# Optimization experiments

Hardware: AMD Instinct MI355X
Metric: run time of the kernel (lower is better)

The kernel has to match this reference:

```python
import jax, jax.numpy as jnp
import numpy as np

V, NLAB, NLAYERS, DI, DM, DS, DD, K = 32000, 9, 2, 768, 1536, 16, 96, 4
B, S = 2, 2048
EPS = 1e-6


def setup_inputs() -> dict:
    key = jax.random.key(0)
    ks = jax.random.split(key, 12)
    n = lambda k, shape, s=0.02: jax.random.normal(k, shape, jnp.float32) * s
    return {
        "input_ids": jax.random.randint(ks[0], (B, S), 0, V, dtype=jnp.int32),
        "attention_mask": jnp.ones((B, S), jnp.int32),
        "emb": n(ks[1], (V, DI)),
        "norm_w": jnp.ones((NLAYERS, DI), jnp.float32),
        "in_proj_w": n(ks[2], (NLAYERS, 2 * DM, DI)),
        "conv_w": n(ks[3], (NLAYERS, DM, K), 0.1),
        "conv_b": jnp.zeros((NLAYERS, DM), jnp.float32),
        "sB_w": n(ks[4], (NLAYERS, DS, DM)),
        "sC_w": n(ks[5], (NLAYERS, DS, DM)),
        "sD1_w": n(ks[6], (NLAYERS, DD, DM)),
        "sD2_w": n(ks[7], (NLAYERS, DM, DD)),
        "A": jnp.tile(jnp.arange(1, DS + 1, dtype=jnp.float32), (NLAYERS, DM, 1)),
        "Dp": jnp.ones((NLAYERS, DM), jnp.float32),
        "out_w": n(ks[8], (NLAYERS, DI, DM)),
        "cls_w": n(ks[9], (NLAB, DI)),
        "cls_b": jnp.zeros((NLAB,), jnp.float32),
    }


def _rmsnorm(x, w):
    return x * jax.lax.rsqrt(jnp.mean(x * x, axis=-1, keepdims=True) + EPS) * w


def _mamba_block(x, norm_w, Wi, cw, cb, WB, WC, W1, W2, A, Dp, Wo):
    # x: (b, l, d_input)
    h = _rmsnorm(x, norm_w)
    a, gate = jnp.split(h @ Wi.T, 2, axis=-1)  # each (b, l, DM)
    # causal depthwise conv1d, kernel K, left-pad K-1 (== Conv1d(pad=K-1)[..., :l])
    L = a.shape[1]
    ap = jnp.pad(a, ((0, 0), (K - 1, 0), (0, 0)))
    conv = cb + sum(ap[:, i:i + L, :] * cw[:, i] for i in range(K))
    a = jax.nn.silu(conv)
    # selective SSM
    Bm = a @ WB.T                                   # (b, l, DS)
    Cm = a @ WC.T                                   # (b, l, DS)
    delta = jax.nn.softplus(Dp + (a @ W1.T) @ W2.T)  # (b, l, DM)
    A_bar = jnp.exp(delta[..., None] * (-A))         # (b, l, DM, DS)
    X_bar = (delta * a)[..., None] * Bm[:, :, None, :]  # (b, l, DM, DS)

    def comb(c1, c2):
        a1, x1 = c1
        a2, x2 = c2
        return a1 * a2, a2 * x1 + x2

    _, hid = jax.lax.associative_scan(comb, (A_bar, X_bar), axis=1)
    y = jnp.einsum('blds,bls->bld', hid, Cm) + Dp * a
    y = y * jax.nn.silu(gate)
    return y @ Wo.T


def _forward(input_ids, attention_mask, emb, norm_w, in_proj_w, conv_w, conv_b,
             sB_w, sC_w, sD1_w, sD2_w, A, Dp, out_w, cls_w, cls_b):
    x = emb[input_ids] * attention_mask[..., None].astype(emb.dtype)
    for i in range(NLAYERS):  # residual Mamba layers
        x = _mamba_block(x, norm_w[i], in_proj_w[i], conv_w[i], conv_b[i],
                         sB_w[i], sC_w[i], sD1_w[i], sD2_w[i], A[i], Dp[i], out_w[i]) + x
    # dropout is identity at inference
    return x @ cls_w.T + cls_b  # logits (b, l, num_labels)


def reference(input_ids, attention_mask, emb, norm_w, in_proj_w, conv_w, conv_b,
              sB_w, sC_w, sD1_w, sD2_w, A, Dp, out_w, cls_w, cls_b):
    return _forward(input_ids, attention_mask, emb, norm_w, in_proj_w, conv_w, conv_b,
                    sB_w, sC_w, sD1_w, sD2_w, A, Dp, out_w, cls_w, cls_b)
```

## Files before the change

kernel.cpp:

```cpp
#include <hip/hip_runtime.h>
#include <hip/hip_bf16.h>
#include <math.h>

#define NLAB 9
#define NL   2
#define DI   768
#define DM   1536
#define DS   16
#define KC   4
#define DD   96
#define BB   2
#define SS   2048
#define TT   (BB*SS)
#define EPSF 1e-6f

#define NCH  32
#define CL   (SS/NCH)

#define NW   128
#define KS   8
#define KSL  (DM/KS)

typedef __attribute__((ext_vector_type(4))) float f32x4;
typedef __attribute__((ext_vector_type(8))) short bf16x8;
typedef __attribute__((ext_vector_type(4))) unsigned short us4;
typedef __attribute__((ext_vector_type(8))) unsigned short us8;

__device__ __forceinline__ float siluf(float x) { return x / (1.f + __expf(-x)); }
__device__ __forceinline__ float softplusf(float x) { return x > 15.f ? x : log1pf(__expf(x)); }

__device__ __forceinline__ unsigned short f2bf(float f) {
    unsigned u = __float_as_uint(f);
    return (unsigned short)((u + 0x7fffu + ((u >> 16) & 1u)) >> 16);
}
__device__ __forceinline__ float bf2f(unsigned short s) {
    return __uint_as_float((unsigned)s << 16);
}

__device__ __forceinline__ void xcd_map(int gx, int gy, int bx, int by,
                                        int& bmt, int& bnt)
{
    int flat = by * gx + bx;
    if ((gx & 1) == 0 && (gy & 3) == 0) {
        int halfx = gx >> 1, quarty = gy >> 2;
        int xcd = flat & 7, local = flat >> 3;
        bnt = (xcd & 1) * halfx + local % halfx;
        bmt = (xcd >> 1) * quarty + local / halfx;
    } else { bmt = by; bnt = bx; }
}

__global__ void f32_to_bf16(const float* __restrict__ src,
                            unsigned short* __restrict__ dst, int n)
{
    int i = (blockIdx.x * 256 + threadIdx.x) * 8;
    if (i >= n) return;
    float4 a = *(const float4*)(src + i);
    float4 b = *(const float4*)(src + i + 4);
    union { unsigned short s[8]; uint4 v; } o;
    o.s[0] = f2bf(a.x); o.s[1] = f2bf(a.y); o.s[2] = f2bf(a.z); o.s[3] = f2bf(a.w);
    o.s[4] = f2bf(b.x); o.s[5] = f2bf(b.y); o.s[6] = f2bf(b.z); o.s[7] = f2bf(b.w);
    *(uint4*)(dst + i) = o.v;
}

__global__ void embed_kernel(const int* __restrict__ ids, const int* __restrict__ mask,
                             const float* __restrict__ emb, float* __restrict__ x)
{
    int t = blockIdx.x;
    int i = threadIdx.x;
    float m = (float)mask[t];
    int id = ids[t];
    float4 v = ((const float4*)(emb + (size_t)id * DI))[i];
    v.x *= m; v.y *= m; v.z *= m; v.w *= m;
    ((float4*)(x + (size_t)t * DI))[i] = v;
}

__global__ void rmsnorm_kernel(const float* __restrict__ x, const float* __restrict__ w,
                               unsigned short* __restrict__ h)
{
    __shared__ float red[4];
    int t = blockIdx.x;
    const float* xr = x + (size_t)t * DI;
    float ss = 0.f;
    for (int i = threadIdx.x; i < DI; i += 256) { float v = xr[i]; ss += v * v; }
    #pragma unroll
    for (int m = 1; m < 64; m <<= 1) ss += __shfl_xor(ss, m, 64);
    if ((threadIdx.x & 63) == 0) red[threadIdx.x >> 6] = ss;
    __syncthreads();
    float scale = rsqrtf((red[0] + red[1] + red[2] + red[3]) * (1.f / DI) + EPSF);
    for (int i = threadIdx.x; i < DI; i += 256)
        h[(size_t)t * DI + i] = f2bf(xr[i] * scale * w[i]);
}

#define STAGE_TILE(AS, BS, KT) do {                                                           \
    _Pragma("unroll")                                                                         \
    for (int it = 0; it < 2; ++it) {                                                          \
        int rbase = it * 64 + wave * 16;                                                      \
        int row = rbase + (lane >> 2);                                                        \
        int c8 = (((lane & 3) ^ ((lane >> 3) & 3)) * 8);                                      \
        __builtin_amdgcn_global_load_lds(                                                     \
            (const __attribute__((address_space(1))) unsigned int*)(Arow + (size_t)row * lda + (KT) + c8), \
            (__attribute__((address_space(3))) unsigned int*)((AS) + rbase * 32), 16, 0, 0);  \
        __builtin_amdgcn_global_load_lds(                                                     \
            (const __attribute__((address_space(1))) unsigned int*)(Brow + (size_t)row * ldb + (KT) + c8), \
            (__attribute__((address_space(3))) unsigned int*)((BS) + rbase * 32), 16, 0, 0);  \
    } } while (0)

#define COMPUTE_TILE(AS, BS) do {                                                             \
    bf16x8 af[4], bfr[4];                                                                     \
    const int khs = (kh ^ ((lr >> 1) & 3)) * 8;                                               \
    _Pragma("unroll")                                                                         \
    for (int i = 0; i < 4; ++i)                                                               \
        af[i] = *(const bf16x8*)&(AS)[(wm + i * 16 + lr) * 32 + khs];                         \
    _Pragma("unroll")                                                                         \
    for (int j = 0; j < 4; ++j)                                                               \
        bfr[j] = *(const bf16x8*)&(BS)[(wn + j * 16 + lr) * 32 + khs];                        \
    _Pragma("unroll")                                                                         \
    for (int i = 0; i < 4; ++i)                                                               \
        _Pragma("unroll")                                                                     \
        for (int j = 0; j < 4; ++j)                                                           \
            acc[i][j] = __builtin_amdgcn_mfma_f32_16x16x32_bf16(af[i], bfr[j], acc[i][j], 0, 0, 0); \
    } while (0)

#define WAIT_BAR(T, NT) do {                                                                  \
    if ((T) + 1 < (NT)) asm volatile("s_waitcnt vmcnt(4)" ::: "memory");                      \
    else                asm volatile("s_waitcnt vmcnt(0)" ::: "memory");                      \
    __builtin_amdgcn_s_barrier();                                                             \
} while (0)

__global__ __launch_bounds__(256) void gemm_bf16(
    const unsigned short* __restrict__ A, const unsigned short* __restrict__ B,
    const float* __restrict__ Rres, const float* __restrict__ bias,
    float* __restrict__ C, int M, int N, int K,
    int lda, int ldb, int ldc, int act, int out16)
{
    __shared__ unsigned short As0[128 * 32];
    __shared__ unsigned short Bs0[128 * 32];
    __shared__ unsigned short As1[128 * 32];
    __shared__ unsigned short Bs1[128 * 32];
    __shared__ unsigned short As2[128 * 32];
    __shared__ unsigned short Bs2[128 * 32];
    const int tid = threadIdx.x;
    const int wave = tid >> 6, lane = tid & 63;

    int bmt, bnt;
    xcd_map(gridDim.x, gridDim.y, blockIdx.x, blockIdx.y, bmt, bnt);
    const int bm = bmt * 128, bn = bnt * 128;

    const int wm = (wave >> 1) * 64, wn = (wave & 1) * 64;
    const int lr = lane & 15, kh = lane >> 4;

    f32x4 acc[4][4] = {};

    const unsigned short* Arow = A + (size_t)bm * lda;
    const unsigned short* Brow = B + (size_t)bn * ldb;

    const int nt = K >> 5;
    STAGE_TILE(As0, Bs0, 0);
    if (nt > 1) STAGE_TILE(As1, Bs1, 32);

    int t = 0;
    while (true) {
        WAIT_BAR(t, nt);
        if (t + 2 < nt) STAGE_TILE(As2, Bs2, (t + 2) * 32);
        COMPUTE_TILE(As0, Bs0);
        if (++t == nt) break;
        WAIT_BAR(t, nt);
        if (t + 2 < nt) STAGE_TILE(As0, Bs0, (t + 2) * 32);
        COMPUTE_TILE(As1, Bs1);
        if (++t == nt) break;
        WAIT_BAR(t, nt);
        if (t + 2 < nt) STAGE_TILE(As1, Bs1, (t + 2) * 32);
        COMPUTE_TILE(As2, Bs2);
        if (++t == nt) break;
    }

    #pragma unroll
    for (int i = 0; i < 4; ++i) {
        #pragma unroll
        for (int j = 0; j < 4; ++j) {
            #pragma unroll
            for (int r = 0; r < 4; ++r) {
                int row = bm + wm + i * 16 + kh * 4 + r;
                int col = bn + wn + j * 16 + lr;
                float v = acc[i][j][r];
                if (bias) v += bias[col];
                if (act == 1) v = softplusf(v);
                if (Rres) v += Rres[(size_t)row * ldc + col];
                if (out16)
                    ((unsigned short*)C)[(size_t)row * ldc + col] = f2bf(v);
                else
                    C[(size_t)row * ldc + col] = v;
            }
        }
    }
}

#define STAGE64(AS, BS, KT) do {                                                              \
    {                                                                                         \
        int rbase = wave * 16;                                                                \
        int row = rbase + (lane >> 2);                                                        \
        int c8 = (((lane & 3) ^ ((lane >> 3) & 3)) * 8);                                      \
        __builtin_amdgcn_global_load_lds(                                                     \
            (const __attribute__((address_space(1))) unsigned int*)(Arow + (size_t)row * DM + (KT) + c8), \
            (__attribute__((address_space(3))) unsigned int*)((AS) + rbase * 32), 16, 0, 0);  \
    }                                                                                         \
    _Pragma("unroll")                                                                         \
    for (int it = 0; it < 2; ++it) {                                                          \
        int rbase = it * 64 + wave * 16;                                                      \
        int row = rbase + (lane >> 2);                                                        \
        int c8 = (((lane & 3) ^ ((lane >> 3) & 3)) * 8);                                      \
        __builtin_amdgcn_global_load_lds(                                                     \
            (const __attribute__((address_space(1))) unsigned int*)(Brow + (size_t)row * DM + (KT) + c8), \
            (__attribute__((address_space(3))) unsigned int*)((BS) + rbase * 32), 16, 0, 0);  \
    } } while (0)

#define COMPUTE64(AS, BS) do {                                                                \
    bf16x8 af[2], bfr[4];                                                                     \
    const int khs = (kh ^ ((lr >> 1) & 3)) * 8;                                               \
    _Pragma("unroll")                                                                         \
    for (int i = 0; i < 2; ++i)                                                               \
        af[i] = *(const bf16x8*)&(AS)[(wm + i * 16 + lr) * 32 + khs];                         \
    _Pragma("unroll")                                                                         \
    for (int j = 0; j < 4; ++j)                                                               \
        bfr[j] = *(const bf16x8*)&(BS)[(wn + j * 16 + lr) * 32 + khs];                        \
    _Pragma("unroll")                                                                         \
    for (int i = 0; i < 2; ++i)                                                               \
        _Pragma("unroll")                                                                     \
        for (int j = 0; j < 4; ++j)                                                           \
            acc[i][j] = __builtin_amdgcn_mfma_f32_16x16x32_bf16(af[i], bfr[j], acc[i][j], 0, 0, 0); \
    } while (0)

#define WAIT_BAR3(T, NT) do {                                                                 \
    if ((T) + 1 < (NT)) asm volatile("s_waitcnt vmcnt(3)" ::: "memory");                      \
    else                asm volatile("s_waitcnt vmcnt(0)" ::: "memory");                      \
    __builtin_amdgcn_s_barrier();                                                             \
} while (0)

__global__ __launch_bounds__(256) void gemm_skinny_bf16(
    const unsigned short* __restrict__ A, const unsigned short* __restrict__ B,
    float* __restrict__ Part)
{
    __shared__ unsigned short As0[64 * 32];
    __shared__ unsigned short Bs0[128 * 32];
    __shared__ unsigned short As1[64 * 32];
    __shared__ unsigned short Bs1[128 * 32];
    __shared__ unsigned short As2[64 * 32];
    __shared__ unsigned short Bs2[128 * 32];
    const int tid = threadIdx.x;
    const int wave = tid >> 6, lane = tid & 63;
    const int bm = blockIdx.x * 64;
    const int ks = blockIdx.y;
    const int k0 = ks * KSL;
    const int wm = (wave >> 1) * 32, wn = (wave & 1) * 64;
    const int lr = lane & 15, kh = lane >> 4;

    f32x4 acc[2][4] = {};

    const unsigned short* Arow = A + (size_t)bm * DM;
    const unsigned short* Brow = B;

    const int nt = KSL >> 5;
    STAGE64(As0, Bs0, k0);
    STAGE64(As1, Bs1, k0 + 32);

    int t = 0;
    while (true) {
        WAIT_BAR3(t, nt);
        if (t + 2 < nt) STAGE64(As2, Bs2, k0 + (t + 2) * 32);
        COMPUTE64(As0, Bs0);
        if (++t == nt) break;
        WAIT_BAR3(t, nt);
        if (t + 2 < nt) STAGE64(As0, Bs0, k0 + (t + 2) * 32);
        COMPUTE64(As1, Bs1);
        if (++t == nt) break;
        WAIT_BAR3(t, nt);
        if (t + 2 < nt) STAGE64(As1, Bs1, k0 + (t + 2) * 32);
        COMPUTE64(As2, Bs2);
        if (++t == nt) break;
    }

    float* out = Part + (size_t)ks * TT * NW;
    #pragma unroll
    for (int i = 0; i < 2; ++i) {
        #pragma unroll
        for (int j = 0; j < 4; ++j) {
            #pragma unroll
            for (int r = 0; r < 4; ++r) {
                int row = bm + wm + i * 16 + kh * 4 + r;
                int col = wn + j * 16 + lr;
                out[(size_t)row * NW + col] = acc[i][j][r];
            }
        }
    }
}

__global__ void skinny_reduce(const float* __restrict__ Part,
                              float* __restrict__ BCD, unsigned short* __restrict__ dd16)
{
    int idx = blockIdx.x * 256 + threadIdx.x;
    float s = 0.f;
    #pragma unroll
    for (int ks = 0; ks < KS; ++ks)
        s += Part[(size_t)ks * TT * NW + idx];
    int col = idx & (NW - 1);
    if (col < 32) BCD[idx] = s;
    else          dd16[(size_t)(idx >> 7) * DD + (col - 32)] = f2bf(s);
}

__global__ __launch_bounds__(256) void delta_kernel(
    const unsigned short* __restrict__ dd16, const unsigned short* __restrict__ W2,
    const float* __restrict__ Dp, float* __restrict__ dtv)
{
    __shared__ unsigned short sdd[16 * DD];
    const int d = blockIdx.x * 256 + threadIdx.x;
    const int t0 = blockIdx.y * 16;

    for (int i = threadIdx.x; i < 16 * DD; i += 256)
        sdd[i] = dd16[(size_t)t0 * DD + i];

    float w[DD];
    {
        const uint4* wp = (const uint4*)(W2 + (size_t)d * DD);
        #pragma unroll
        for (int i = 0; i < DD / 8; ++i) {
            uint4 v = wp[i];
            const unsigned short* ps = (const unsigned short*)&v;
            #pragma unroll
            for (int e = 0; e < 8; ++e) w[i * 8 + e] = bf2f(ps[e]);
        }
    }
    float dpd = Dp[d];
    __syncthreads();

    for (int tt = 0; tt < 16; ++tt) {
        float acc = dpd;
        #pragma unroll
        for (int kk = 0; kk < DD / 8; ++kk) {
            us8 dv = *(const us8*)&sdd[tt * DD + kk * 8];
            #pragma unroll
            for (int e = 0; e < 8; ++e)
                acc += bf2f(dv[e]) * w[kk * 8 + e];
        }
        dtv[(size_t)(t0 + tt) * DM + d] = softplusf(acc);
    }
}

__global__ __launch_bounds__(192) void conv_silu_kernel(
    const unsigned short* __restrict__ proj16, const float* __restrict__ cw,
    const float* __restrict__ cb, unsigned short* __restrict__ aconv16)
{
    int t = blockIdx.x;
    int d0 = threadIdx.x * 8;
    int p = t & (SS - 1);

    float4 w[8];
    #pragma unroll
    for (int k = 0; k < 8; ++k) w[k] = ((const float4*)cw)[d0 + k];
    float acc[8];
    #pragma unroll
    for (int k = 0; k < 8; ++k) acc[k] = cb[d0 + k];

    #pragma unroll
    for (int j = 0; j < KC; ++j) {
        int pp = p - (KC - 1) + j;
        if (pp >= 0) {
            const unsigned short* rowp = proj16 + (size_t)(t - (KC - 1) + j) * (2 * DM) + d0;
            us4 lo = *(const us4*)rowp;
            us4 hi = *(const us4*)(rowp + 4);
            #pragma unroll
            for (int k = 0; k < 4; ++k) {
                acc[k]     += (&w[k].x)[j]     * bf2f(lo[k]);
                acc[4 + k] += (&w[4 + k].x)[j] * bf2f(hi[k]);
            }
        }
    }
    union { unsigned short s[8]; uint4 v; } o;
    #pragma unroll
    for (int k = 0; k < 8; ++k) o.s[k] = f2bf(siluf(acc[k]));
    *(uint4*)(aconv16 + (size_t)t * DM + d0) = o.v;
}

__global__ void concat_w_kernel(const float* __restrict__ WB, const float* __restrict__ WC,
                                const float* __restrict__ W1, unsigned short* __restrict__ Wcat16)
{
    int l = blockIdx.y;
    int row = blockIdx.x;
    const float* src;
    if (row < 16)      src = WB + (size_t)l * DS * DM + (size_t)row * DM;
    else if (row < 32) src = WC + (size_t)l * DS * DM + (size_t)(row - 16) * DM;
    else               src = W1 + (size_t)l * DD * DM + (size_t)(row - 32) * DM;
    unsigned short* dst = Wcat16 + ((size_t)l * NW + row) * DM;
    for (int i = threadIdx.x; i < DM / 4; i += 256) {
        float4 v = ((const float4*)src)[i];
        us4 u = { f2bf(v.x), f2bf(v.y), f2bf(v.z), f2bf(v.w) };
        *(us4*)(dst + i * 4) = u;
    }
}

__global__ __launch_bounds__(256) void scan_pass1(
    const float* __restrict__ dtv, const unsigned short* __restrict__ av16,
    const float* __restrict__ BCD, const float* __restrict__ Amat,
    float2* __restrict__ PQ)
{
    __shared__ float4 sB4[CL][DS / 4];
    int b = blockIdx.z, c = blockIdx.y;
    int d = blockIdx.x * 256 + threadIdx.x;
    size_t rowbase = (size_t)b * SS + (size_t)c * CL;

    for (int i = threadIdx.x; i < CL * DS; i += 256)
        ((float*)sB4)[i] = BCD[(rowbase + (i >> 4)) * NW + (i & 15)];
    __syncthreads();

    float negA[DS], hid[DS];
    #pragma unroll
    for (int s = 0; s < DS; ++s) {
        negA[s] = -Amat[(size_t)d * DS + s];
        hid[s] = 0.f;
    }
    float cum = 0.f;

    const float* pd = dtv + rowbase * DM + d;
    const unsigned short* pa = av16 + rowbase * DM + d;
    for (int t = 0; t < CL; ++t) {
        float dt = pd[(size_t)t * DM];
        float avv = bf2f(pa[(size_t)t * DM]);
        cum += dt;
        float xv = dt * avv;
        #pragma unroll
        for (int j = 0; j < DS / 4; ++j) {
            float4 bv = sB4[t][j];
            hid[4*j+0] = __expf(dt * negA[4*j+0]) * hid[4*j+0] + xv * bv.x;
            hid[4*j+1] = __expf(dt * negA[4*j+1]) * hid[4*j+1] + xv * bv.y;
            hid[4*j+2] = __expf(dt * negA[4*j+2]) * hid[4*j+2] + xv * bv.z;
            hid[4*j+3] = __expf(dt * negA[4*j+3]) * hid[4*j+3] + xv * bv.w;
        }
    }
    float2* out = PQ + ((size_t)(b * NCH + c) * DM + d) * DS;
    #pragma unroll
    for (int s = 0; s < DS; ++s)
        out[s] = make_float2(__expf(cum * negA[s]), hid[s]);
}

__global__ void scan_carry(float2* __restrict__ PQ)
{
    int idx = blockIdx.x * 256 + threadIdx.x;
    int b = idx / (DM * DS);
    int r = idx - b * (DM * DS);
    float2* base = PQ + (size_t)b * NCH * (DM * DS) + r;
    float carry = 0.f;
    for (int cb = 0; cb < NCH; cb += 8) {
        float2 v[8];
        #pragma unroll
        for (int j = 0; j < 8; ++j)
            v[j] = base[(size_t)(cb + j) * (DM * DS)];
        #pragma unroll
        for (int j = 0; j < 8; ++j) {
            base[(size_t)(cb + j) * (DM * DS)].x = carry;
            carry = v[j].x * carry + v[j].y;
        }
    }
}

__global__ __launch_bounds__(256) void scan_pass2(
    const float* __restrict__ dtv, const unsigned short* __restrict__ av16,
    const float* __restrict__ BCD,
    const unsigned short* __restrict__ proj16, const float* __restrict__ Amat,
    const float* __restrict__ Dp, const float2* __restrict__ PQ,
    unsigned short* __restrict__ y)
{
    __shared__ float4 sB4[CL][DS / 4];
    __shared__ float4 sC4[CL][DS / 4];
    int b = blockIdx.z, c = blockIdx.y;
    int d = blockIdx.x * 256 + threadIdx.x;
    size_t rowbase = (size_t)b * SS + (size_t)c * CL;

    for (int i = threadIdx.x; i < CL * DS; i += 256) {
        size_t row = rowbase + (i >> 4);
        ((float*)sB4)[i] = BCD[row * NW + (i & 15)];
        ((float*)sC4)[i] = BCD[row * NW + 16 + (i & 15)];
    }
    __syncthreads();

    float negA[DS], hid[DS];
    const float2* pin = PQ + ((size_t)(b * NCH + c) * DM + d) * DS;
    #pragma unroll
    for (int s = 0; s < DS; ++s) {
        negA[s] = -Amat[(size_t)d * DS + s];
        hid[s] = pin[s].x;
    }
    float Dpd = Dp[d];

    const float* pd = dtv + rowbase * DM + d;
    const unsigned short* pa = av16 + rowbase * DM + d;
    const unsigned short* gp = proj16 + rowbase * (2 * DM) + DM + d;
    unsigned short* yp = y + rowbase * DM + d;

    for (int t = 0; t < CL; ++t) {
        float dt = pd[(size_t)t * DM];
        float avv = bf2f(pa[(size_t)t * DM]);
        float g  = bf2f(gp[(size_t)t * (2 * DM)]);
        float xv = dt * avv;
        float acc0 = 0.f, acc1 = 0.f, acc2 = 0.f, acc3 = 0.f;
        #pragma unroll
        for (int j = 0; j < DS / 4; ++j) {
            float4 bv = sB4[t][j];
            float4 cv = sC4[t][j];
            hid[4*j+0] = __expf(dt * negA[4*j+0]) * hid[4*j+0] + xv * bv.x;
            hid[4*j+1] = __expf(dt * negA[4*j+1]) * hid[4*j+1] + xv * bv.y;
            hid[4*j+2] = __expf(dt * negA[4*j+2]) * hid[4*j+2] + xv * bv.z;
            hid[4*j+3] = __expf(dt * negA[4*j+3]) * hid[4*j+3] + xv * bv.w;
            acc0 += hid[4*j+0] * cv.x;
            acc1 += hid[4*j+1] * cv.y;
            acc2 += hid[4*j+2] * cv.z;
            acc3 += hid[4*j+3] * cv.w;
        }
        float contrib = (acc0 + acc1) + (acc2 + acc3);
        yp[(size_t)t * DM] = f2bf((contrib + Dpd * avv) * siluf(g));
    }
}

__global__ __launch_bounds__(256) void cls_kernel(
    const float* __restrict__ x, const float* __restrict__ W,
    const float* __restrict__ bias, float* __restrict__ out)
{
    int t = blockIdx.x * 4 + (threadIdx.x >> 6);
    int lane = threadIdx.x & 63;
    const float* xr = x + (size_t)t * DI;
    float acc[NLAB];
    #pragma unroll
    for (int n = 0; n < NLAB; ++n) acc[n] = 0.f;
    for (int i = lane; i < DI; i += 64) {
        float xv = xr[i];
        #pragma unroll
        for (int n = 0; n < NLAB; ++n) acc[n] += xv * W[(size_t)n * DI + i];
    }
    #pragma unroll
    for (int n = 0; n < NLAB; ++n)
        #pragma unroll
        for (int m = 1; m < 64; m <<= 1) acc[n] += __shfl_xor(acc[n], m, 64);
    if (lane < NLAB) out[(size_t)t * NLAB + lane] = acc[lane] + bias[lane];
}

extern "C" void kernel_launch(void* const* d_in, const int* in_sizes, int n_in,
                              void* d_out, int out_size, void* d_ws, size_t ws_size,
                              hipStream_t stream)
{
    const int*   ids    = (const int*)d_in[0];
    const int*   mask   = (const int*)d_in[1];
    const float* emb    = (const float*)d_in[2];
    const float* norm_w = (const float*)d_in[3];
    const float* Wi     = (const float*)d_in[4];
    const float* conv_w = (const float*)d_in[5];
    const float* conv_b = (const float*)d_in[6];
    const float* sB_w   = (const float*)d_in[7];
    const float* sC_w   = (const float*)d_in[8];
    const float* sD1_w  = (const float*)d_in[9];
    const float* sD2_w  = (const float*)d_in[10];
    const float* Amat   = (const float*)d_in[11];
    const float* Dp     = (const float*)d_in[12];
    const float* out_w  = (const float*)d_in[13];
    const float* cls_w  = (const float*)d_in[14];
    const float* cls_b  = (const float*)d_in[15];
    float* logits = (float*)d_out;

    float* ws = (float*)d_ws;
    size_t off = 0;
    float* x     = ws + off; off += (size_t)TT * DI;
    unsigned short* proj16 = (unsigned short*)(ws + off); off += (size_t)TT * 2 * DM / 2;
    float* dtv   = ws + off; off += (size_t)TT * DM;
    float* BCD   = ws + off; off += (size_t)TT * NW;
    size_t scratch_sz = (size_t)BB * NCH * DM * DS * 2;
    size_t part_sz = (size_t)KS * TT * NW;
    if (part_sz > scratch_sz) scratch_sz = part_sz;
    float* Part  = ws + off;
    float2* PQ   = (float2*)(ws + off); off += scratch_sz;
    unsigned short* y16     = (unsigned short*)(ws + off); off += (size_t)TT * DM / 2;
    unsigned short* aconv16 = (unsigned short*)(ws + off); off += (size_t)TT * DM / 2;
    unsigned short* Wi16    = (unsigned short*)(ws + off); off += (size_t)NL * 2 * DM * DI / 2;
    unsigned short* Wo16    = (unsigned short*)(ws + off); off += (size_t)NL * DI * DM / 2;
    unsigned short* W216    = (unsigned short*)(ws + off); off += (size_t)NL * DM * DD / 2;
    unsigned short* dd16    = (unsigned short*)(ws + off); off += (size_t)TT * DD / 2;
    unsigned short* Wcat16  = (unsigned short*)(ws + off); off += (size_t)NL * NW * DM / 2;
    if (ws_size < off * sizeof(float)) return;

    unsigned short* h16 = (unsigned short*)dtv;

    embed_kernel<<<TT, DI / 4, 0, stream>>>(ids, mask, emb, x);
    concat_w_kernel<<<dim3(NW, NL), 256, 0, stream>>>(sB_w, sC_w, sD1_w, Wcat16);

    f32_to_bf16<<<(NL * 2 * DM * DI / 8 + 255) / 256, 256, 0, stream>>>(Wi, Wi16, NL * 2 * DM * DI);
    f32_to_bf16<<<(NL * DI * DM / 8 + 255) / 256, 256, 0, stream>>>(out_w, Wo16, NL * DI * DM);
    f32_to_bf16<<<(NL * DM * DD / 8 + 255) / 256, 256, 0, stream>>>(sD2_w, W216, NL * DM * DD);

    for (int l = 0; l < NL; ++l) {
        const float* cw_l  = conv_w + (size_t)l * DM * KC;
        const float* cb_l  = conv_b + (size_t)l * DM;
        const float* A_l   = Amat  + (size_t)l * DM * DS;
        const float* Dp_l  = Dp    + (size_t)l * DM;
        const float* nw_l  = norm_w + (size_t)l * DI;
        const unsigned short* Wi16_l  = Wi16  + (size_t)l * 2 * DM * DI;
        const unsigned short* Wo16_l  = Wo16  + (size_t)l * DI * DM;
        const unsigned short* W216_l  = W216  + (size_t)l * DM * DD;
        const unsigned short* Wcat16_l = Wcat16 + (size_t)l * NW * DM;

        rmsnorm_kernel<<<TT, 256, 0, stream>>>(x, nw_l, h16);

        gemm_bf16<<<dim3(2 * DM / 128, TT / 128), 256, 0, stream>>>(
            h16, Wi16_l, nullptr, nullptr, (float*)proj16, TT, 2 * DM, DI, DI, DI, 2 * DM, 0, 1);

        conv_silu_kernel<<<TT, DM / 8, 0, stream>>>(proj16, cw_l, cb_l, aconv16);

        gemm_skinny_bf16<<<dim3(TT / 64, KS), 256, 0, stream>>>(aconv16, Wcat16_l, Part);
        skinny_reduce<<<TT * NW / 256, 256, 0, stream>>>(Part, BCD, dd16);

        delta_kernel<<<dim3(DM / 256, TT / 16), 256, 0, stream>>>(dd16, W216_l, Dp_l, dtv);

        scan_pass1<<<dim3(DM / 256, NCH, BB), 256, 0, stream>>>(dtv, aconv16, BCD, A_l, PQ);
        scan_carry<<<BB * DM * DS / 256, 256, 0, stream>>>(PQ);
        scan_pass2<<<dim3(DM / 256, NCH, BB), 256, 0, stream>>>(
            dtv, aconv16, BCD, proj16, A_l, Dp_l, PQ, y16);

        gemm_bf16<<<dim3(DI / 128, TT / 128), 256, 0, stream>>>(
            y16, Wo16_l, x, nullptr, x, TT, DI, DM, DM, DM, DI, 0, 0);
    }

    cls_kernel<<<TT / 4, 256, 0, stream>>>(x, cls_w, cls_b, logits);
}
```

Measured before the change: 762.0 us.

## Swap GEMM tile shapes, double scan chunks, vectorize rmsnorm, reshape cls launch

The main GEMM now uses 64x128 tiles instead of 128x128, which doubles the block count for the in-proj and out-proj GEMMs. The skinny GEMM goes the other way, to 128-row tiles. The scan chunk count rises from 32 to 64 to add parallelism in the chunked scan. rmsnorm now uses one float4 per thread with 192 threads, and cls_kernel launches one 64-thread block per token. The aim is better occupancy and wave balance, at the cost of less reuse per block in the main GEMMs and more carry work in the scan.

```diff
diff --git a/kernel.cpp b/kernel.cpp
--- a/kernel.cpp
+++ b/kernel.cpp
@@ -14,7 +14,7 @@
 #define TT   (BB*SS)
 #define EPSF 1e-6f
 
-#define NCH  32
+#define NCH  64
 #define CL   (SS/NCH)
 
 #define NW   128
@@ -74,55 +74,62 @@
     ((float4*)(x + (size_t)t * DI))[i] = v;
 }
 
-__global__ void rmsnorm_kernel(const float* __restrict__ x, const float* __restrict__ w,
-                               unsigned short* __restrict__ h)
-{
-    __shared__ float red[4];
+__global__ __launch_bounds__(192) void rmsnorm_kernel(
+    const float* __restrict__ x, const float* __restrict__ w,
+    unsigned short* __restrict__ h)
+{
+    __shared__ float red[3];
     int t = blockIdx.x;
-    const float* xr = x + (size_t)t * DI;
-    float ss = 0.f;
-    for (int i = threadIdx.x; i < DI; i += 256) { float v = xr[i]; ss += v * v; }
+    float4 v = ((const float4*)(x + (size_t)t * DI))[threadIdx.x];
+    float ss = v.x * v.x + v.y * v.y + v.z * v.z + v.w * v.w;
     #pragma unroll
     for (int m = 1; m < 64; m <<= 1) ss += __shfl_xor(ss, m, 64);
     if ((threadIdx.x & 63) == 0) red[threadIdx.x >> 6] = ss;
     __syncthreads();
-    float scale = rsqrtf((red[0] + red[1] + red[2] + red[3]) * (1.f / DI) + EPSF);
-    for (int i = threadIdx.x; i < DI; i += 256)
-        h[(size_t)t * DI + i] = f2bf(xr[i] * scale * w[i]);
-}
-
-#define STAGE_TILE(AS, BS, KT) do {                                                           \
+    float scale = rsqrtf((red[0] + red[1] + red[2]) * (1.f / DI) + EPSF);
+    float4 wv = ((const float4*)w)[threadIdx.x];
+    us4 o = { f2bf(v.x * scale * wv.x), f2bf(v.y * scale * wv.y),
+              f2bf(v.z * scale * wv.z), f2bf(v.w * scale * wv.w) };
+    *(us4*)(h + (size_t)t * DI + threadIdx.x * 4) = o;
+}
+
+#define STAGE_T64(AS, BS, KT) do {                                                            \
+    {                                                                                         \
+        int rbase = wave * 16;                                                                \
+        int row = rbase + (lane >> 2);                                                        \
+        int c8 = (((lane & 3) ^ ((lane >> 3) & 3)) * 8);                                      \
+        __builtin_amdgcn_global_load_lds(                                                     \
+            (const __attribute__((address_space(1))) unsigned int*)(Arow + (size_t)row * lda + (KT) + c8), \
+            (__attribute__((address_space(3))) unsigned int*)((AS) + rbase * 32), 16, 0, 0);  \
+    }                                                                                         \
     _Pragma("unroll")                                                                         \
     for (int it = 0; it < 2; ++it) {                                                          \
         int rbase = it * 64 + wave * 16;                                                      \
         int row = rbase + (lane >> 2);                                                        \
         int c8 = (((lane & 3) ^ ((lane >> 3) & 3)) * 8);                                      \
         __builtin_amdgcn_global_load_lds(                                                     \
-            (const __attribute__((address_space(1))) unsigned int*)(Arow + (size_t)row * lda + (KT) + c8), \
-            (__attribute__((address_space(3))) unsigned int*)((AS) + rbase * 32), 16, 0, 0);  \
-        __builtin_amdgcn_global_load_lds(                                                     \
             (const __attribute__((address_space(1))) unsigned int*)(Brow + (size_t)row * ldb + (KT) + c8), \
             (__attribute__((address_space(3))) unsigned int*)((BS) + rbase * 32), 16, 0, 0);  \
     } } while (0)
 
-#define COMPUTE_TILE(AS, BS) do {                                                             \
-    bf16x8 af[4], bfr[4];                                                                     \
+#define COMPUTE_T64(AS, BS) do {                                                              \
+    bf16x8 af[2], bfr[4];                                                                     \
     const int khs = (kh ^ ((lr >> 1) & 3)) * 8;                                               \
     _Pragma("unroll")                                                                         \
-    for (int i = 0; i < 4; ++i)                                                               \
+    for (int i = 0; i < 2; ++i)                                                               \
         af[i] = *(const bf16x8*)&(AS)[(wm + i * 16 + lr) * 32 + khs];                         \
     _Pragma("unroll")                                                                         \
     for (int j = 0; j < 4; ++j)                                                               \
         bfr[j] = *(const bf16x8*)&(BS)[(wn + j * 16 + lr) * 32 + khs];                        \
     _Pragma("unroll")                                                                         \
-    for (int i = 0; i < 4; ++i)                                                               \
+    for (int i = 0; i < 2; ++i)                                                               \
         _Pragma("unroll")                                                                     \
         for (int j = 0; j < 4; ++j)                                                           \
             acc[i][j] = __builtin_amdgcn_mfma_f32_16x16x32_bf16(af[i], bfr[j], acc[i][j], 0, 0, 0); \
     } while (0)
 
-#define WAIT_BAR(T, NT) do {                                                                  \
-    if ((T) + 1 < (NT)) asm volatile("s_waitcnt vmcnt(4)" ::: "memory");                      \
+#define WAIT_BAR3(T, NT) do {                                                                 \
+    if ((T) + 1 < (NT)) asm volatile("s_waitcnt vmcnt(3)" ::: "memory");                      \
     else                asm volatile("s_waitcnt vmcnt(0)" ::: "memory");                      \
     __builtin_amdgcn_s_barrier();                                                             \
 } while (0)
@@ -133,49 +140,49 @@
     float* __restrict__ C, int M, int N, int K,
     int lda, int ldb, int ldc, int act, int out16)
 {
-    __shared__ unsigned short As0[128 * 32];
+    __shared__ unsigned short As0[64 * 32];
     __shared__ unsigned short Bs0[128 * 32];
-    __shared__ unsigned short As1[128 * 32];
+    __shared__ unsigned short As1[64 * 32];
     __shared__ unsigned short Bs1[128 * 32];
-    __shared__ unsigned short As2[128 * 32];
+    __shared__ unsigned short As2[64 * 32];
     __shared__ unsigned short Bs2[128 * 32];
     const int tid = threadIdx.x;
     const int wave = tid >> 6, lane = tid & 63;
 
     int bmt, bnt;
     xcd_map(gridDim.x, gridDim.y, blockIdx.x, blockIdx.y, bmt, bnt);
-    const int bm = bmt * 128, bn = bnt * 128;
-
-    const int wm = (wave >> 1) * 64, wn = (wave & 1) * 64;
+    const int bm = bmt * 64, bn = bnt * 128;
+
+    const int wm = (wave >> 1) * 32, wn = (wave & 1) * 64;
     const int lr = lane & 15, kh = lane >> 4;
 
-    f32x4 acc[4][4] = {};
+    f32x4 acc[2][4] = {};
 
     const unsigned short* Arow = A + (size_t)bm * lda;
     const unsigned short* Brow = B + (size_t)bn * ldb;
 
     const int nt = K >> 5;
-    STAGE_TILE(As0, Bs0, 0);
-    if (nt > 1) STAGE_TILE(As1, Bs1, 32);
+    STAGE_T64(As0, Bs0, 0);
+    STAGE_T64(As1, Bs1, 32);
 
     int t = 0;
     while (true) {
-        WAIT_BAR(t, nt);
-        if (t + 2 < nt) STAGE_TILE(As2, Bs2, (t + 2) * 32);
-        COMPUTE_TILE(As0, Bs0);
+        WAIT_BAR3(t, nt);
+        if (t + 2 < nt) STAGE_T64(As2, Bs2, (t + 2) * 32);
+        COMPUTE_T64(As0, Bs0);
         if (++t == nt) break;
-        WAIT_BAR(t, nt);
-        if (t + 2 < nt) STAGE_TILE(As0, Bs0, (t + 2) * 32);
-        COMPUTE_TILE(As1, Bs1);
+        WAIT_BAR3(t, nt);
+        if (t + 2 < nt) STAGE_T64(As0, Bs0, (t + 2) * 32);
+        COMPUTE_T64(As1, Bs1);
         if (++t == nt) break;
-        WAIT_BAR(t, nt);
-        if (t + 2 < nt) STAGE_TILE(As1, Bs1, (t + 2) * 32);
-        COMPUTE_TILE(As2, Bs2);
+        WAIT_BAR3(t, nt);
+        if (t + 2 < nt) STAGE_T64(As1, Bs1, (t + 2) * 32);
+        COMPUTE_T64(As2, Bs2);
         if (++t == nt) break;
     }
 
     #pragma unroll
-    for (int i = 0; i < 4; ++i) {
+    for (int i = 0; i < 2; ++i) {
         #pragma unroll
         for (int j = 0; j < 4; ++j) {
             #pragma unroll
@@ -195,43 +202,38 @@
     }
 }
 
-#define STAGE64(AS, BS, KT) do {                                                              \
-    {                                                                                         \
-        int rbase = wave * 16;                                                                \
-        int row = rbase + (lane >> 2);                                                        \
-        int c8 = (((lane & 3) ^ ((lane >> 3) & 3)) * 8);                                      \
-        __builtin_amdgcn_global_load_lds(                                                     \
-            (const __attribute__((address_space(1))) unsigned int*)(Arow + (size_t)row * DM + (KT) + c8), \
-            (__attribute__((address_space(3))) unsigned int*)((AS) + rbase * 32), 16, 0, 0);  \
-    }                                                                                         \
+#define STAGE_TILE(AS, BS, KT) do {                                                           \
     _Pragma("unroll")                                                                         \
     for (int it = 0; it < 2; ++it) {                                                          \
         int rbase = it * 64 + wave * 16;                                                      \
         int row = rbase + (lane >> 2);                                                        \
         int c8 = (((lane & 3) ^ ((lane >> 3) & 3)) * 8);                                      \
         __builtin_amdgcn_global_load_lds(                                                     \
-            (const __attribute__((address_space(1))) unsigned int*)(Brow + (size_t)row * DM + (KT) + c8), \
+            (const __attribute__((address_space(1))) unsigned int*)(Arow + (size_t)row * lda + (KT) + c8), \
+            (__attribute__((address_space(3))) unsigned int*)((AS) + rbase * 32), 16, 0, 0);  \
+        __builtin_amdgcn_global_load_lds(                                                     \
+            (const __attribute__((address_space(1))) unsigned int*)(Brow + (size_t)row * ldb + (KT) + c8), \
             (__attribute__((address_space(3))) unsigned int*)((BS) + rbase * 32), 16, 0, 0);  \
     } } while (0)
 
-#define COMPUTE64(AS, BS) do {                                                                \
-    bf16x8 af[2], bfr[4];                                                                     \
+#define COMPUTE_TILE(AS, BS) do {                                                             \
+    bf16x8 af[4], bfr[4];                                                                     \
     const int khs = (kh ^ ((lr >> 1) & 3)) * 8;                                               \
     _Pragma("unroll")                                                                         \
-    for (int i = 0; i < 2; ++i)                                                               \
+    for (int i = 0; i < 4; ++i)                                                               \
         af[i] = *(const bf16x8*)&(AS)[(wm + i * 16 + lr) * 32 + khs];                         \
     _Pragma("unroll")                                                                         \
     for (int j = 0; j < 4; ++j)                                                               \
         bfr[j] = *(const bf16x8*)&(BS)[(wn + j * 16 + lr) * 32 + khs];                        \
     _Pragma("unroll")                                                                         \
-    for (int i = 0; i < 2; ++i)                                                               \
+    for (int i = 0; i < 4; ++i)                                                               \
         _Pragma("unroll")                                                                     \
         for (int j = 0; j < 4; ++j)                                                           \
             acc[i][j] = __builtin_amdgcn_mfma_f32_16x16x32_bf16(af[i], bfr[j], acc[i][j], 0, 0, 0); \
     } while (0)
 
-#define WAIT_BAR3(T, NT) do {                                                                 \
-    if ((T) + 1 < (NT)) asm volatile("s_waitcnt vmcnt(3)" ::: "memory");                      \
+#define WAIT_BAR(T, NT) do {                                                                  \
+    if ((T) + 1 < (NT)) asm volatile("s_waitcnt vmcnt(4)" ::: "memory");                      \
     else                asm volatile("s_waitcnt vmcnt(0)" ::: "memory");                      \
     __builtin_amdgcn_s_barrier();                                                             \
 } while (0)
@@ -240,48 +242,49 @@
     const unsigned short* __restrict__ A, const unsigned short* __restrict__ B,
     float* __restrict__ Part)
 {
-    __shared__ unsigned short As0[64 * 32];
+    __shared__ unsigned short As0[128 * 32];
     __shared__ unsigned short Bs0[128 * 32];
-    __shared__ unsigned short As1[64 * 32];
+    __shared__ unsigned short As1[128 * 32];
     __shared__ unsigned short Bs1[128 * 32];
-    __shared__ unsigned short As2[64 * 32];
+    __shared__ unsigned short As2[128 * 32];
     __shared__ unsigned short Bs2[128 * 32];
     const int tid = threadIdx.x;
     const int wave = tid >> 6, lane = tid & 63;
-    const int bm = blockIdx.x * 64;
+    const int bm = blockIdx.x * 128;
     const int ks = blockIdx.y;
     const int k0 = ks * KSL;
-    const int wm = (wave >> 1) * 32, wn = (wave & 1) * 64;
+    const int wm = (wave >> 1) * 64, wn = (wave & 1) * 64;
     const int lr = lane & 15, kh = lane >> 4;
-
-    f32x4 acc[2][4] = {};
+    const int lda = DM, ldb = DM;
+
+    f32x4 acc[4][4] = {};
 
     const unsigned short* Arow = A + (size_t)bm * DM;
     const unsigned short* Brow = B;
 
     const int nt = KSL >> 5;
-    STAGE64(As0, Bs0, k0);
-    STAGE64(As1, Bs1, k0 + 32);
+    STAGE_TILE(As0, Bs0, k0);
+    STAGE_TILE(As1, Bs1, k0 + 32);
 
     int t = 0;
     while (true) {
-        WAIT_BAR3(t, nt);
-        if (t + 2 < nt) STAGE64(As2, Bs2, k0 + (t + 2) * 32);
-        COMPUTE64(As0, Bs0);
+        WAIT_BAR(t, nt);
+        if (t + 2 < nt) STAGE_TILE(As2, Bs2, k0 + (t + 2) * 32);
+        COMPUTE_TILE(As0, Bs0);
         if (++t == nt) break;
-        WAIT_BAR3(t, nt);
-        if (t + 2 < nt) STAGE64(As0, Bs0, k0 + (t + 2) * 32);
-        COMPUTE64(As1, Bs1);
+        WAIT_BAR(t, nt);
+        if (t + 2 < nt) STAGE_TILE(As0, Bs0, k0 + (t + 2) * 32);
+        COMPUTE_TILE(As1, Bs1);
         if (++t == nt) break;
-        WAIT_BAR3(t, nt);
-        if (t + 2 < nt) STAGE64(As1, Bs1, k0 + (t + 2) * 32);
-        COMPUTE64(As2, Bs2);
+        WAIT_BAR(t, nt);
+        if (t + 2 < nt) STAGE_TILE(As1, Bs1, k0 + (t + 2) * 32);
+        COMPUTE_TILE(As2, Bs2);
         if (++t == nt) break;
     }
 
     float* out = Part + (size_t)ks * TT * NW;
     #pragma unroll
-    for (int i = 0; i < 2; ++i) {
+    for (int i = 0; i < 4; ++i) {
         #pragma unroll
         for (int j = 0; j < 4; ++j) {
             #pragma unroll
@@ -519,12 +522,11 @@
     }
 }
 
-__global__ __launch_bounds__(256) void cls_kernel(
-    const float* __restrict__ x, const float* __restrict__ W,
-    const float* __restrict__ bias, float* __restrict__ out)
-{
-    int t = blockIdx.x * 4 + (threadIdx.x >> 6);
-    int lane = threadIdx.x & 63;
+__global__ void cls_kernel(const float* __restrict__ x, const float* __restrict__ W,
+                           const float* __restrict__ bias, float* __restrict__ out)
+{
+    int t = blockIdx.x;
+    int lane = threadIdx.x;
     const float* xr = x + (size_t)t * DI;
     float acc[NLAB];
     #pragma unroll
@@ -603,14 +605,14 @@
         const unsigned short* W216_l  = W216  + (size_t)l * DM * DD;
         const unsigned short* Wcat16_l = Wcat16 + (size_t)l * NW * DM;
 
-        rmsnorm_kernel<<<TT, 256, 0, stream>>>(x, nw_l, h16);
-
-        gemm_bf16<<<dim3(2 * DM / 128, TT / 128), 256, 0, stream>>>(
+        rmsnorm_kernel<<<TT, DI / 4, 0, stream>>>(x, nw_l, h16);
+
+        gemm_bf16<<<dim3(2 * DM / 128, TT / 64), 256, 0, stream>>>(
             h16, Wi16_l, nullptr, nullptr, (float*)proj16, TT, 2 * DM, DI, DI, DI, 2 * DM, 0, 1);
 
         conv_silu_kernel<<<TT, DM / 8, 0, stream>>>(proj16, cw_l, cb_l, aconv16);
 
-        gemm_skinny_bf16<<<dim3(TT / 64, KS), 256, 0, stream>>>(aconv16, Wcat16_l, Part);
+        gemm_skinny_bf16<<<dim3(TT / 128, KS), 256, 0, stream>>>(aconv16, Wcat16_l, Part);
         skinny_reduce<<<TT * NW / 256, 256, 0, stream>>>(Part, BCD, dd16);
 
         delta_kernel<<<dim3(DM / 256, TT / 16), 256, 0, stream>>>(dd16, W216_l, Dp_l, dtv);
@@ -620,9 +622,9 @@
         scan_pass2<<<dim3(DM / 256, NCH, BB), 256, 0, stream>>>(
             dtv, aconv16, BCD, proj16, A_l, Dp_l, PQ, y16);
 
-        gemm_bf16<<<dim3(DI / 128, TT / 128), 256, 0, stream>>>(
+        gemm_bf16<<<dim3(DI / 128, TT / 64), 256, 0, stream>>>(
             y16, Wo16_l, x, nullptr, x, TT, DI, DM, DM, DM, DI, 0, 0);
     }
 
-    cls_kernel<<<TT / 4, 256, 0, stream>>>(x, cls_w, cls_b, logits);
-}
+    cls_kernel<<<TT, 64, 0, stream>>>(x, cls_w, cls_b, logits);
+}
```

Measured after the change: 677.5 us. 11.1% less time.
